# Kernel optimization log

Measured on AMD Instinct MI355X. Metric: run time of the kernel, lower is better.

## Reference

```python
import jax, jax.numpy as jnp
import numpy as np

B, S, HID = 1, 4096, 2048
H, HKV, D = 16, 4, 128
BLOCK = 32          # dllm_block_length
EPS = 1e-6
SCALE = D ** -0.5


def setup_inputs() -> dict:
    key = jax.random.key(0)
    ks = jax.random.split(key, 4)
    hidden_states = jax.random.normal(ks[0], (B, S, HID), dtype=jnp.float32)
    # RoPE tables (interleaved-half convention), shape [S, D]
    inv_freq = 1.0 / (10000.0 ** (np.arange(0, D, 2, dtype=np.float32) / D))
    t = np.arange(S, dtype=np.float32)
    freqs = np.outer(t, inv_freq)                      # [S, D/2]
    emb = np.concatenate([freqs, freqs], axis=-1)      # [S, D]
    cos = jnp.asarray(np.cos(emb), dtype=jnp.float32)
    sin = jnp.asarray(np.sin(emb), dtype=jnp.float32)
    w_qkv = jax.random.normal(ks[1], (HID, (H + 2 * HKV) * D), dtype=jnp.float32) * (HID ** -0.5)
    w_o = jax.random.normal(ks[2], (H * D, HID), dtype=jnp.float32) * ((H * D) ** -0.5)
    q_norm_w = jnp.ones((D,), dtype=jnp.float32)
    k_norm_w = jnp.ones((D,), dtype=jnp.float32)
    return {"hidden_states": hidden_states, "cos": cos, "sin": sin,
            "w_qkv": w_qkv, "q_norm_w": q_norm_w, "k_norm_w": k_norm_w, "w_o": w_o}


def _rms_norm(x, w):
    var = jnp.mean(jnp.square(x), axis=-1, keepdims=True)
    return x * jax.lax.rsqrt(var + EPS) * w


def _rotate_half(x):
    x1, x2 = jnp.split(x, 2, axis=-1)
    return jnp.concatenate([-x2, x1], axis=-1)


def reference(hidden_states, cos, sin, w_qkv, q_norm_w, k_norm_w, w_o):
    b, s, _ = hidden_states.shape
    qkv = hidden_states @ w_qkv                                   # [B,S,(H+2Hkv)*D]
    q = qkv[..., : H * D].reshape(b, s, H, D)
    k = qkv[..., H * D: (H + HKV) * D].reshape(b, s, HKV, D)
    v = qkv[..., (H + HKV) * D:].reshape(b, s, HKV, D)
    # per-head RMSNorm on q/k (use_qk_norm)
    q = _rms_norm(q, q_norm_w)
    k = _rms_norm(k, k_norm_w)
    # RoPE
    c = cos[None, :, None, :]
    sn = sin[None, :, None, :]
    q = q * c + _rotate_half(q) * sn
    k = k * c + _rotate_half(k) * sn
    # GQA: repeat kv heads
    rep = H // HKV
    k = jnp.repeat(k, rep, axis=2)                                # [B,S,H,D]
    v = jnp.repeat(v, rep, axis=2)
    scores = jnp.einsum("bshd,bthd->bhst", q, k) * SCALE          # [B,H,S,S]
    # block-diffusion mask: bidirectional within a dllm block, causal across blocks
    blk = jnp.arange(s) // BLOCK
    allowed = blk[None, :] <= blk[:, None]                        # [S,S]
    scores = jnp.where(allowed[None, None], scores, jnp.finfo(scores.dtype).min)
    attn = jax.nn.softmax(scores, axis=-1)
    out = jnp.einsum("bhst,bthd->bshd", attn, v).reshape(b, s, H * D)
    return out @ w_o
```

## Files before the change

kernel.cpp:

```cpp
#include <hip/hip_runtime.h>
#include <cstdint>

typedef __bf16 bf16;
typedef __attribute__((ext_vector_type(4))) __bf16 bf16x4;
typedef __attribute__((ext_vector_type(8))) __bf16 bf16x8;
typedef __attribute__((ext_vector_type(4))) float f32x4;

#define MFMA16(a, b, c) __builtin_amdgcn_mfma_f32_16x16x32_bf16((a), (b), (c), 0, 0, 0)

static __device__ __forceinline__ void gload16(const void* g, void* l) {
  __builtin_amdgcn_global_load_lds(
      (const __attribute__((address_space(1))) void*)g,
      (__attribute__((address_space(3))) void*)l, 16, 0, 0);
}

#define SWZ128(r, k) ((r) * 128 + ((k) ^ (((r) & 7) << 3)))
#define SWZP(r, k)   ((r) * 64  + ((k) ^ (((r) & 7) << 3)))
#define SWZV(r, k)   ((r) * 64  + ((k) ^ (((r) & 7) << 3)))

__global__ __launch_bounds__(256) void k_convert(const float* __restrict__ in,
                                                 bf16* __restrict__ out, int n4) {
  int i = blockIdx.x * blockDim.x + threadIdx.x;
  if (i >= n4) return;
  float4 v = *(const float4*)&in[(size_t)i * 4];
  bf16x4 o;
  o[0] = (bf16)v.x; o[1] = (bf16)v.y; o[2] = (bf16)v.z; o[3] = (bf16)v.w;
  *(bf16x4*)&out[(size_t)i * 4] = o;
}

__global__ void k_transpose(const float* __restrict__ in, bf16* __restrict__ out,
                            int R, int C) {
  __shared__ float tile[32][33];
  int bx = blockIdx.x, by = blockIdx.y;
  int tx = threadIdx.x, ty = threadIdx.y;
#pragma unroll
  for (int i = ty; i < 32; i += 8)
    tile[i][tx] = in[(size_t)(by * 32 + i) * C + bx * 32 + tx];
  __syncthreads();
#pragma unroll
  for (int i = ty; i < 32; i += 8)
    out[(size_t)(bx * 32 + i) * R + by * 32 + tx] = (bf16)tile[tx][i];
}

__global__ void k_vtrans(const bf16* __restrict__ qkv, bf16* __restrict__ vtg) {
  __shared__ bf16 tile[32][33];
  int s0 = blockIdx.x * 32, d0 = blockIdx.y * 32, hk = blockIdx.z;
  int tx = threadIdx.x, ty = threadIdx.y;
#pragma unroll
  for (int i = ty; i < 32; i += 8)
    tile[i][tx] = qkv[(size_t)(s0 + i) * 3072 + 2560 + hk * 128 + d0 + tx];
  __syncthreads();
#pragma unroll
  for (int i = ty; i < 32; i += 8)
    vtg[(size_t)hk * 524288 + (size_t)(d0 + i) * 4096 + s0 + tx] = tile[tx][i];
}

template <typename OutT>
__global__ __launch_bounds__(256) void k_gemm(const bf16* __restrict__ A,
                                              const bf16* __restrict__ BT,
                                              OutT* __restrict__ C, int M, int N, int K) {
  __shared__ bf16 As[128 * 32];
  __shared__ bf16 Bs[128 * 32];
  const int tid = threadIdx.x;
  const int wv = tid >> 6, lane = tid & 63;
  const int lr = lane & 15, lg = lane >> 4;
  const int wm = (wv >> 1) * 64, wn = (wv & 1) * 64;
  const int bm = blockIdx.x, bn = blockIdx.y;
  const size_t baseA = (size_t)bm * 128 * K;
  const size_t baseB = (size_t)bn * 128 * K;
  f32x4 acc[4][4] = {};
  for (int kt = 0; kt < K; kt += 32) {
    __syncthreads();
#pragma unroll
    for (int inst = 0; inst < 2; ++inst) {
      int ch = inst * 256 + tid;
      int row = ch >> 2, ko = (ch & 3) * 8;
      gload16(A + baseA + (size_t)row * K + kt + ko, &As[(size_t)(inst * 256 + wv * 64) * 8]);
      gload16(BT + baseB + (size_t)row * K + kt + ko, &Bs[(size_t)(inst * 256 + wv * 64) * 8]);
    }
    __syncthreads();
    bf16x8 af[4], bfr[4];
#pragma unroll
    for (int mi = 0; mi < 4; ++mi) af[mi] = *(const bf16x8*)&As[(wm + mi * 16 + lr) * 32 + lg * 8];
#pragma unroll
    for (int nj = 0; nj < 4; ++nj) bfr[nj] = *(const bf16x8*)&Bs[(wn + nj * 16 + lr) * 32 + lg * 8];
#pragma unroll
    for (int mi = 0; mi < 4; ++mi)
#pragma unroll
      for (int nj = 0; nj < 4; ++nj)
        acc[mi][nj] = MFMA16(af[mi], bfr[nj], acc[mi][nj]);
  }
#pragma unroll
  for (int mi = 0; mi < 4; ++mi)
#pragma unroll
    for (int nj = 0; nj < 4; ++nj)
#pragma unroll
      for (int j = 0; j < 4; ++j) {
        int r = bm * 128 + wm + mi * 16 + lg * 4 + j;
        int c = bn * 128 + wn + nj * 16 + lr;
        C[(size_t)r * N + c] = (OutT)acc[mi][nj][j];
      }
}

__global__ __launch_bounds__(256) void k_rmsrope(bf16* __restrict__ qkv,
                                                 const float* __restrict__ cosb,
                                                 const float* __restrict__ sinb,
                                                 const float* __restrict__ qw,
                                                 const float* __restrict__ kw) {
  int row = blockIdx.x * 4 + (threadIdx.x >> 6);
  int lane = threadIdx.x & 63;
  int s = row / 20, hd = row % 20;
  bool isq = hd < 16;
  int col = isq ? hd * 128 : 2048 + (hd - 16) * 128;
  bf16* p = qkv + (size_t)s * 3072 + col;
  float x1 = (float)p[lane], x2 = (float)p[lane + 64];
  float ss = x1 * x1 + x2 * x2;
#pragma unroll
  for (int m = 32; m; m >>= 1) ss += __shfl_xor(ss, m);
  float r = rsqrtf(ss * (1.0f / 128.0f) + 1e-6f);
  const float* w = isq ? qw : kw;
  float y1 = x1 * r * w[lane], y2 = x2 * r * w[lane + 64];
  float c1 = cosb[s * 128 + lane], c2 = cosb[s * 128 + lane + 64];
  float s1 = sinb[s * 128 + lane], s2 = sinb[s * 128 + lane + 64];
  p[lane] = (bf16)(y1 * c1 - y2 * s1);
  p[lane + 64] = (bf16)(y2 * c2 + y1 * s2);
}

__global__ __launch_bounds__(512, 2) void k_attn(const bf16* __restrict__ qkv,
                                                 const bf16* __restrict__ vtg,
                                                 bf16* __restrict__ out) {
  __shared__ bf16 Ks[64 * 128];
  __shared__ bf16 Pl[128 * 64];
  __shared__ bf16 Vt[128 * 64];
  const int tid = threadIdx.x;
  const int wv = tid >> 6, lane = tid & 63;
  const int lr = lane & 15, lg = lane >> 4;
  const int u = blockIdx.x & 255, vsl = blockIdx.x >> 8;
  const int h = u & 15;
  const int qa = u >> 4;
  const int qt = vsl ? (31 - qa) : qa;
  const int q0 = qt * 128;
  const int hk = h >> 2;
  const int wq = wv * 16;
  const float K2 = 0.12751744f;

  const int chK0 = tid, chK1 = 512 + tid;
  const int rowK0 = chK0 >> 4, rowK1 = chK1 >> 4;
  const int doffK0 = ((chK0 & 15) * 8) ^ ((rowK0 & 7) << 3);
  const int doffK1 = ((chK1 & 15) * 8) ^ ((rowK1 & 7) << 3);
  const int drow0 = chK0 >> 3, drow1 = chK1 >> 3;
  const int koffV0 = ((chK0 & 7) * 8) ^ ((drow0 & 7) << 3);
  const int koffV1 = ((chK1 & 7) * 8) ^ ((drow1 & 7) << 3);
  const bf16* kb0 = qkv + 2048 + hk * 128 + doffK0;
  const bf16* kb1 = qkv + 2048 + hk * 128 + doffK1;
  const bf16* vb0 = vtg + (size_t)hk * 524288 + (size_t)drow0 * 4096 + koffV0;
  const bf16* vb1 = vtg + (size_t)hk * 524288 + (size_t)drow1 * 4096 + koffV1;

  bf16x8 qf[4];
  {
    const bf16* qrow = qkv + (size_t)(q0 + wq + lr) * 3072 + h * 128 + lg * 8;
#pragma unroll
    for (int kk = 0; kk < 4; ++kk) qf[kk] = *(const bf16x8*)(qrow + kk * 32);
  }

  f32x4 oacc[8] = {};
  float mst = -1e30f, lst = 0.f;
  const int lim = (wq + lr) | 31;

  const int nkb = 2 * qt + 2;

  for (int kb = 0; kb < nkb; ++kb) {
    const int t0 = kb * 64;
    __syncthreads();
    gload16(kb0 + (size_t)(t0 + rowK0) * 3072, &Ks[(size_t)(wv * 64) * 8]);
    gload16(kb1 + (size_t)(t0 + rowK1) * 3072, &Ks[(size_t)(512 + wv * 64) * 8]);
    gload16(vb0 + t0, &Vt[(size_t)(wv * 64) * 8]);
    gload16(vb1 + t0, &Vt[(size_t)(512 + wv * 64) * 8]);
    __syncthreads();

    f32x4 sacc[4] = {};
    __builtin_amdgcn_s_setprio(1);
#pragma unroll
    for (int kk = 0; kk < 4; ++kk) {
      bf16x8 bk[4];
#pragma unroll
      for (int a = 0; a < 4; ++a)
        bk[a] = *(const bf16x8*)&Ks[SWZ128(a * 16 + lr, kk * 32 + lg * 8)];
#pragma unroll
      for (int a = 0; a < 4; ++a)
        sacc[a] = MFMA16(bk[a], qf[kk], sacc[a]);
    }
    __builtin_amdgcn_s_setprio(0);

    const bool maskt = (kb >= 2 * qt);
    const int koff2 = (kb - 2 * qt) * 64;
    float rm = -1e30f;
#pragma unroll
    for (int a = 0; a < 4; ++a)
#pragma unroll
      for (int j = 0; j < 4; ++j) {
        float sv = sacc[a][j] * K2;
        if (maskt && (koff2 + a * 16 + lg * 4 + j > lim)) sv = -1e30f;
        sacc[a][j] = sv;
        rm = fmaxf(rm, sv);
      }
    rm = fmaxf(rm, __shfl_xor(rm, 16));
    rm = fmaxf(rm, __shfl_xor(rm, 32));
    if (__any(rm - mst > 8.0f)) {
      float mnew = fmaxf(mst, rm);
      float al = exp2f(mst - mnew);
      mst = mnew;
      lst *= al;
      float alo[4];
#pragma unroll
      for (int j = 0; j < 4; ++j) alo[j] = __shfl(al, lg * 4 + j);
#pragma unroll
      for (int dj = 0; dj < 8; ++dj)
#pragma unroll
        for (int j = 0; j < 4; ++j) oacc[dj][j] *= alo[j];
    }
    float rs = 0.f;
#pragma unroll
    for (int a = 0; a < 4; ++a) {
      bf16x4 pw;
#pragma unroll
      for (int j = 0; j < 4; ++j) {
        float p = exp2f(sacc[a][j] - mst);
        rs += p;
        pw[j] = (bf16)p;
      }
      *(bf16x4*)&Pl[SWZP(wq + lr, a * 16 + lg * 4)] = pw;
    }
    rs += __shfl_xor(rs, 16);
    rs += __shfl_xor(rs, 32);
    lst += rs;

    __builtin_amdgcn_s_setprio(1);
#pragma unroll
    for (int kk = 0; kk < 2; ++kk) {
      bf16x8 ap = *(const bf16x8*)&Pl[SWZP(wq + lr, kk * 32 + lg * 8)];
#pragma unroll
      for (int dj = 0; dj < 8; ++dj) {
        bf16x8 bv = *(const bf16x8*)&Vt[SWZV(dj * 16 + lr, kk * 32 + lg * 8)];
        oacc[dj] = MFMA16(ap, bv, oacc[dj]);
      }
    }
    __builtin_amdgcn_s_setprio(0);
  }

  float lrec = 1.0f / lst;
  float linv[4];
#pragma unroll
  for (int j = 0; j < 4; ++j) linv[j] = __shfl(lrec, lg * 4 + j);
#pragma unroll
  for (int dj = 0; dj < 8; ++dj)
#pragma unroll
    for (int j = 0; j < 4; ++j) {
      int srow = q0 + wq + lg * 4 + j;
      int d = dj * 16 + lr;
      out[(size_t)srow * 2048 + h * 128 + d] = (bf16)(oacc[dj][j] * linv[j]);
    }
}

extern "C" void kernel_launch(void* const* d_in, const int* in_sizes, int n_in,
                              void* d_out, int out_size, void* d_ws, size_t ws_size,
                              hipStream_t stream) {
  const float* hs = (const float*)d_in[0];
  const float* cosb = (const float*)d_in[1];
  const float* sinb = (const float*)d_in[2];
  const float* w_qkv = (const float*)d_in[3];
  const float* qw = (const float*)d_in[4];
  const float* kw = (const float*)d_in[5];
  const float* w_o = (const float*)d_in[6];
  float* out = (float*)d_out;

  char* ws = (char*)d_ws;
  bf16* qkv   = (bf16*)(ws);
  bf16* hsb   = (bf16*)(ws + 25165824);
  bf16* wqkvT = (bf16*)(ws + 41943040);
  bf16* woT   = (bf16*)(ws + 41943040);
  bf16* attno = (bf16*)(ws + 25165824);
  bf16* vtg   = (bf16*)(ws + 54525952);

  k_convert<<<8192, 256, 0, stream>>>(hs, hsb, 2097152);
  k_transpose<<<dim3(96, 64), dim3(32, 8), 0, stream>>>(w_qkv, wqkvT, 2048, 3072);
  k_gemm<bf16><<<dim3(32, 24), 256, 0, stream>>>(hsb, wqkvT, qkv, 4096, 3072, 2048);
  k_rmsrope<<<20480, 256, 0, stream>>>(qkv, cosb, sinb, qw, kw);
  k_vtrans<<<dim3(128, 4, 4), dim3(32, 8), 0, stream>>>(qkv, vtg);
  k_transpose<<<dim3(64, 64), dim3(32, 8), 0, stream>>>(w_o, woT, 2048, 2048);
  k_attn<<<512, 512, 0, stream>>>(qkv, vtg, attno);
  k_gemm<float><<<dim3(32, 16), 256, 0, stream>>>(attno, woT, out, 4096, 2048, 2048);
}
```

Measured before the change: 315.9 us.

## Split long causal attention tiles across two blocks with a combine kernel

Attention query tiles 16-31, the ones with the most key blocks, are now split into two halves over the key range and run as separate workgroups. Each half writes a normalized partial output plus its running max and sum, and a new combine kernel merges the two halves with softmax weights. Grid size goes from 512 to 768 to balance work across CUs. The s_setprio hints are removed, and the change adds a kernel launch plus extra partial-output traffic through global memory.

Result: faster. 292.7 us (-7.3%).

```diff
diff --git a/kernel.cpp b/kernel.cpp
--- a/kernel.cpp
+++ b/kernel.cpp
@@ -128,17 +128,30 @@
 
 __global__ __launch_bounds__(512, 2) void k_attn(const bf16* __restrict__ qkv,
                                                  const bf16* __restrict__ vtg,
-                                                 bf16* __restrict__ out) {
+                                                 bf16* __restrict__ out,
+                                                 bf16* __restrict__ pO,
+                                                 float2* __restrict__ pml) {
   __shared__ bf16 Ks[64 * 128];
   __shared__ bf16 Pl[128 * 64];
   __shared__ bf16 Vt[128 * 64];
   const int tid = threadIdx.x;
   const int wv = tid >> 6, lane = tid & 63;
   const int lr = lane & 15, lg = lane >> 4;
-  const int u = blockIdx.x & 255, vsl = blockIdx.x >> 8;
-  const int h = u & 15;
-  const int qa = u >> 4;
-  const int qt = vsl ? (31 - qa) : qa;
+  const int b = blockIdx.x;
+  int h, qt, kb0, kb1, tile = 0, half = 0;
+  bool split;
+  if (b < 256) {
+    h = b & 15; qt = b >> 4; kb0 = 0; kb1 = 2 * qt + 2; split = false;
+  } else {
+    half = (b >= 512);
+    int u = b - (half ? 512 : 256);
+    h = u & 15; qt = 31 - (u >> 4);
+    tile = h * 16 + (qt - 16);
+    const int nh = qt + 1;
+    kb0 = half ? nh : 0;
+    kb1 = half ? 2 * qt + 2 : nh;
+    split = true;
+  }
   const int q0 = qt * 128;
   const int hk = h >> 2;
   const int wq = wv * 16;
@@ -151,8 +164,8 @@
   const int drow0 = chK0 >> 3, drow1 = chK1 >> 3;
   const int koffV0 = ((chK0 & 7) * 8) ^ ((drow0 & 7) << 3);
   const int koffV1 = ((chK1 & 7) * 8) ^ ((drow1 & 7) << 3);
-  const bf16* kb0 = qkv + 2048 + hk * 128 + doffK0;
-  const bf16* kb1 = qkv + 2048 + hk * 128 + doffK1;
+  const bf16* kb0p = qkv + 2048 + hk * 128 + doffK0;
+  const bf16* kb1p = qkv + 2048 + hk * 128 + doffK1;
   const bf16* vb0 = vtg + (size_t)hk * 524288 + (size_t)drow0 * 4096 + koffV0;
   const bf16* vb1 = vtg + (size_t)hk * 524288 + (size_t)drow1 * 4096 + koffV1;
 
@@ -167,19 +180,16 @@
   float mst = -1e30f, lst = 0.f;
   const int lim = (wq + lr) | 31;
 
-  const int nkb = 2 * qt + 2;
-
-  for (int kb = 0; kb < nkb; ++kb) {
+  for (int kb = kb0; kb < kb1; ++kb) {
     const int t0 = kb * 64;
     __syncthreads();
-    gload16(kb0 + (size_t)(t0 + rowK0) * 3072, &Ks[(size_t)(wv * 64) * 8]);
-    gload16(kb1 + (size_t)(t0 + rowK1) * 3072, &Ks[(size_t)(512 + wv * 64) * 8]);
+    gload16(kb0p + (size_t)(t0 + rowK0) * 3072, &Ks[(size_t)(wv * 64) * 8]);
+    gload16(kb1p + (size_t)(t0 + rowK1) * 3072, &Ks[(size_t)(512 + wv * 64) * 8]);
     gload16(vb0 + t0, &Vt[(size_t)(wv * 64) * 8]);
     gload16(vb1 + t0, &Vt[(size_t)(512 + wv * 64) * 8]);
     __syncthreads();
 
     f32x4 sacc[4] = {};
-    __builtin_amdgcn_s_setprio(1);
 #pragma unroll
     for (int kk = 0; kk < 4; ++kk) {
       bf16x8 bk[4];
@@ -190,7 +200,6 @@
       for (int a = 0; a < 4; ++a)
         sacc[a] = MFMA16(bk[a], qf[kk], sacc[a]);
     }
-    __builtin_amdgcn_s_setprio(0);
 
     const bool maskt = (kb >= 2 * qt);
     const int koff2 = (kb - 2 * qt) * 64;
@@ -235,7 +244,6 @@
     rs += __shfl_xor(rs, 32);
     lst += rs;
 
-    __builtin_amdgcn_s_setprio(1);
 #pragma unroll
     for (int kk = 0; kk < 2; ++kk) {
       bf16x8 ap = *(const bf16x8*)&Pl[SWZP(wq + lr, kk * 32 + lg * 8)];
@@ -245,21 +253,62 @@
         oacc[dj] = MFMA16(ap, bv, oacc[dj]);
       }
     }
-    __builtin_amdgcn_s_setprio(0);
   }
 
   float lrec = 1.0f / lst;
   float linv[4];
 #pragma unroll
   for (int j = 0; j < 4; ++j) linv[j] = __shfl(lrec, lg * 4 + j);
-#pragma unroll
-  for (int dj = 0; dj < 8; ++dj)
-#pragma unroll
-    for (int j = 0; j < 4; ++j) {
-      int srow = q0 + wq + lg * 4 + j;
-      int d = dj * 16 + lr;
-      out[(size_t)srow * 2048 + h * 128 + d] = (bf16)(oacc[dj][j] * linv[j]);
-    }
+  if (!split) {
+#pragma unroll
+    for (int dj = 0; dj < 8; ++dj)
+#pragma unroll
+      for (int j = 0; j < 4; ++j) {
+        int srow = q0 + wq + lg * 4 + j;
+        int d = dj * 16 + lr;
+        out[(size_t)srow * 2048 + h * 128 + d] = (bf16)(oacc[dj][j] * linv[j]);
+      }
+  } else {
+    if (lg == 0) pml[((size_t)half * 256 + tile) * 128 + wq + lr] = make_float2(mst, lst);
+    bf16* pb = pO + (((size_t)half * 256 + tile) * 128) * 128;
+#pragma unroll
+    for (int dj = 0; dj < 8; ++dj)
+#pragma unroll
+      for (int j = 0; j < 4; ++j) {
+        int row = wq + lg * 4 + j;
+        int d = dj * 16 + lr;
+        pb[(size_t)row * 128 + d] = (bf16)(oacc[dj][j] * linv[j]);
+      }
+  }
+}
+
+__global__ __launch_bounds__(256) void k_comb(const bf16* __restrict__ pO,
+                                              const float2* __restrict__ pml,
+                                              bf16* __restrict__ attno) {
+  const int tile = blockIdx.x;
+  const int h = tile >> 4, qt = 16 + (tile & 15);
+  const int t = threadIdx.x;
+  const int r = blockIdx.y * 32 + (t >> 3);
+  const int d0 = (t & 7) * 16;
+  float2 m0 = pml[(size_t)tile * 128 + r];
+  float2 m1 = pml[(size_t)(256 + tile) * 128 + r];
+  float mm = fmaxf(m0.x, m1.x);
+  float w0 = m0.y * exp2f(m0.x - mm);
+  float w1 = m1.y * exp2f(m1.x - mm);
+  float inv = 1.0f / (w0 + w1);
+  w0 *= inv; w1 *= inv;
+  const bf16* p0 = pO + ((size_t)tile * 128 + r) * 128 + d0;
+  const bf16* p1 = pO + ((size_t)(256 + tile) * 128 + r) * 128 + d0;
+  bf16* o = attno + (size_t)(qt * 128 + r) * 2048 + h * 128 + d0;
+#pragma unroll
+  for (int v = 0; v < 2; ++v) {
+    bf16x8 a = *(const bf16x8*)(p0 + v * 8);
+    bf16x8 c = *(const bf16x8*)(p1 + v * 8);
+    bf16x8 ov;
+#pragma unroll
+    for (int i = 0; i < 8; ++i) ov[i] = (bf16)((float)a[i] * w0 + (float)c[i] * w1);
+    *(bf16x8*)(o + v * 8) = ov;
+  }
 }
 
 extern "C" void kernel_launch(void* const* d_in, const int* in_sizes, int n_in,
@@ -281,6 +330,8 @@
   bf16* woT   = (bf16*)(ws + 41943040);
   bf16* attno = (bf16*)(ws + 25165824);
   bf16* vtg   = (bf16*)(ws + 54525952);
+  bf16* pO    = (bf16*)(ws + 58720256);
+  float2* pml = (float2*)(ws + 75497472);
 
   k_convert<<<8192, 256, 0, stream>>>(hs, hsb, 2097152);
   k_transpose<<<dim3(96, 64), dim3(32, 8), 0, stream>>>(w_qkv, wqkvT, 2048, 3072);
@@ -288,6 +339,7 @@
   k_rmsrope<<<20480, 256, 0, stream>>>(qkv, cosb, sinb, qw, kw);
   k_vtrans<<<dim3(128, 4, 4), dim3(32, 8), 0, stream>>>(qkv, vtg);
   k_transpose<<<dim3(64, 64), dim3(32, 8), 0, stream>>>(w_o, woT, 2048, 2048);
-  k_attn<<<512, 512, 0, stream>>>(qkv, vtg, attno);
+  k_attn<<<768, 512, 0, stream>>>(qkv, vtg, attno, pO, pml);
+  k_comb<<<dim3(256, 4), 256, 0, stream>>>(pO, pml, attno);
   k_gemm<float><<<dim3(32, 16), 256, 0, stream>>>(attno, woT, out, 4096, 2048, 2048);
 }
```
